# Kernel tuning notes

Measured on AMD Instinct MI355X. Metric: run time of the kernel, lower is better.

The kernel has to match this reference:

```python
import jax, jax.numpy as jnp
import numpy as np

NH = 12
D = 768
HD = D // NH
F = 3072
EPS = 1e-6
SCALE = 1.0 / np.sqrt(HD).astype(np.float32)


def _ln(x, g, b):
    m = x.mean(-1, keepdims=True)
    v = ((x - m) ** 2).mean(-1, keepdims=True)
    return (x - m) / jnp.sqrt(v + EPS) * g + b


def _heads(t):
    B, S, _ = t.shape
    return t.reshape(B, S, NH, HD).transpose(0, 2, 1, 3)  # [B,H,S,hd]


def _attn(q, k, v):
    # q,k,v: [B,H,S,hd]; dropout rate is 0 so omitted
    s = jnp.einsum('bhqd,bhkd->bhqk', q, k) * SCALE
    p = jax.nn.softmax(s, axis=-1)
    c = jnp.einsum('bhqk,bhkd->bhqd', p, v)
    B, H, S, _ = c.shape
    return c.transpose(0, 2, 1, 3).reshape(B, S, D)


def _mlp(x, W1, b1, W2, b2):
    h = jax.nn.gelu(x @ W1 + b1)  # dropout rate 0.1 -> identity (eval)
    return h @ W2 + b2


def setup_inputs() -> dict:
    key = jax.random.key(0)
    ks = jax.random.split(key, 16)
    B, S = 4, 1024
    rnd = lambda k, sh: (jax.random.normal(k, sh, jnp.float32) * 0.02)
    inp = {
        'x': jax.random.normal(ks[0], (B, S, D), jnp.float32),
        'y': jax.random.normal(ks[1], (B, S, D), jnp.float32),
        'ln1x_g': jnp.ones((D,)), 'ln1x_b': jnp.zeros((D,)),
        'ln1y_g': jnp.ones((D,)), 'ln1y_b': jnp.zeros((D,)),
        'Wq': rnd(ks[2], (D, D)), 'bq': jnp.zeros((D,)),
        'Wk': rnd(ks[3], (D, D)), 'bk': jnp.zeros((D,)),
        'Wv': rnd(ks[4], (D, D)), 'bv': jnp.zeros((D,)),
        'Wo': rnd(ks[5], (D, D)), 'bo': jnp.zeros((D,)),
        'Wqd': rnd(ks[6], (D, D)), 'bqd': jnp.zeros((D,)),
        'Wkd': rnd(ks[7], (D, D)), 'bkd': jnp.zeros((D,)),
        'Wvd': rnd(ks[8], (D, D)), 'bvd': jnp.zeros((D,)),
        'Wod': rnd(ks[9], (D, D)), 'bod': jnp.zeros((D,)),
        'w11': jnp.full((1,), 0.5), 'w12': jnp.full((1,), 0.5),
        'w21': jnp.full((1,), 0.5), 'w22': jnp.full((1,), 0.5),
        'ln2x_g': jnp.ones((D,)), 'ln2x_b': jnp.zeros((D,)),
        'ln2y_g': jnp.ones((D,)), 'ln2y_b': jnp.zeros((D,)),
        'W1': rnd(ks[10], (D, F)), 'b1': jnp.zeros((F,)),
        'W2': rnd(ks[11], (F, D)), 'b2': jnp.zeros((D,)),
        'W1d': rnd(ks[12], (D, F)), 'b1d': jnp.zeros((F,)),
        'W2d': rnd(ks[13], (F, D)), 'b2d': jnp.zeros((D,)),
    }
    return inp


def reference(x, y, ln1x_g, ln1x_b, ln1y_g, ln1y_b,
              Wq, bq, Wk, bk, Wv, bv, Wo, bo,
              Wqd, bqd, Wkd, bkd, Wvd, bvd, Wod, bod,
              w11, w12, w21, w22,
              ln2x_g, ln2x_b, ln2y_g, ln2y_b,
              W1, b1, W2, b2, W1d, b1d, W2d, b2d):
    hx, hy = x, y
    xn = _ln(x, ln1x_g, ln1x_b)
    yn = _ln(y, ln1y_g, ln1y_b)
    q = _heads(xn @ Wq + bq); k = _heads(xn @ Wk + bk); v = _heads(xn @ Wv + bv)
    qd = _heads(yn @ Wqd + bqd); kd = _heads(yn @ Wkd + bkd); vd = _heads(yn @ Wvd + bvd)
    a_sx = _attn(q, k, v) @ Wo + bo          # self-x
    a_sy = _attn(qd, kd, vd) @ Wod + bod     # self-y
    a_cx = _attn(q, kd, vd) @ Wo + bo        # cross x-query into y
    a_cy = _attn(qd, k, v) @ Wod + bod       # cross y-query into x
    ax = w11 * a_sx + w12 * a_cx
    ay = w21 * a_sy + w22 * a_cy
    x = ax + hx
    y = ay + hy
    hx, hy = x, y
    x = _mlp(_ln(x, ln2x_g, ln2x_b), W1, b1, W2, b2) + hx
    y = _mlp(_ln(y, ln2y_g, ln2y_b), W1d, b1d, W2d, b2d) + hy
    return (x, y)
```

## Files before the change

kernel.cpp:

```cpp
#include <hip/hip_runtime.h>

typedef unsigned short u16;
typedef unsigned short u16x8 __attribute__((ext_vector_type(8)));
typedef short s16x8 __attribute__((ext_vector_type(8)));
typedef float f32x4 __attribute__((ext_vector_type(4)));

#define EL ((size_t)3145728)
#define DDE ((size_t)589824)
#define DFE ((size_t)2359296)

#if __has_builtin(__builtin_amdgcn_exp2f)
#define EXP2(x) __builtin_amdgcn_exp2f(x)
#else
#define EXP2(x) __expf((x) * 0.6931471805599453f)
#endif

__device__ __forceinline__ float b2f(u16 u) {
    return __builtin_bit_cast(float, (unsigned)u << 16);
}
__device__ __forceinline__ u16 f2bf(float f) {
    unsigned x = __builtin_bit_cast(unsigned, f);
    return (u16)((x + 0x7fffu + ((x >> 16) & 1u)) >> 16);
}
__device__ __forceinline__ float gelu_f(float x) {
    float t = x + 0.044715f * x * x * x;
    return x * __builtin_amdgcn_rcpf(1.0f + EXP2(-2.302207417f * t));
}
__device__ __forceinline__ f32x4 mfma16(s16x8 a, s16x8 b, f32x4 c) {
    return __builtin_amdgcn_mfma_f32_16x16x32_bf16(a, b, c, 0, 0, 0);
}
__device__ __forceinline__ void gld16(const u16* g, u16* l) {
    __builtin_amdgcn_global_load_lds((const __attribute__((address_space(1))) void*)g,
                                     (__attribute__((address_space(3))) void*)l,
                                     16, 0, 0);
}
__device__ __forceinline__ void xcd_map(int NN, int& m, int& n, int& z) {
    int p = blockIdx.x, T = gridDim.x;
    int ppx = T >> 3;
    int xcd = p & 7, l = p >> 3;
    int panel = l / NN;
    n = l - panel * NN;
    int gp = xcd * (ppx / NN) + panel;
    z = gp >> 5;
    m = gp & 31;
}

__global__ __launch_bounds__(256) void transpose8_k(const float* p0, const float* p1,
                                                    const float* p2, const float* p3,
                                                    const float* p4, const float* p5,
                                                    const float* p6, const float* p7,
                                                    u16* __restrict__ dst0) {
    int z = blockIdx.z;
    const float* in = z == 0 ? p0 : z == 1 ? p1 : z == 2 ? p2 : z == 3 ? p3
                    : z == 4 ? p4 : z == 5 ? p5 : z == 6 ? p6 : p7;
    u16* out = dst0 + (size_t)z * DDE;
    const int K = 768, N = 768;
    __shared__ u16 tile[64][72];
    int k0 = blockIdx.y << 6, n0 = blockIdx.x << 6;
    int tid = threadIdx.x;
    int r = tid >> 2, c = (tid & 3) << 4;
    const float* ip = in + (size_t)(k0 + r) * N + n0 + c;
#pragma unroll
    for (int q = 0; q < 4; ++q) {
        f32x4 v = *(const f32x4*)(ip + 4 * q);
#pragma unroll
        for (int e = 0; e < 4; ++e) tile[r][c + 4 * q + e] = f2bf(v[e]);
    }
    __syncthreads();
    u16x8 o0, o1;
#pragma unroll
    for (int e = 0; e < 8; ++e) { o0[e] = tile[c + e][r]; o1[e] = tile[c + 8 + e][r]; }
    u16* op = out + (size_t)(n0 + r) * K + k0 + c;
    *(u16x8*)op = o0;
    *(u16x8*)(op + 8) = o1;
}

__global__ __launch_bounds__(256) void transpose2_k(const float* pa, const float* pb,
                                                    u16* __restrict__ dst0, size_t dsz,
                                                    int K, int N) {
    int z = blockIdx.z;
    const float* in = z ? pb : pa;
    u16* out = dst0 + (size_t)z * dsz;
    __shared__ u16 tile[64][72];
    int k0 = blockIdx.y << 6, n0 = blockIdx.x << 6;
    int tid = threadIdx.x;
    int r = tid >> 2, c = (tid & 3) << 4;
    const float* ip = in + (size_t)(k0 + r) * N + n0 + c;
#pragma unroll
    for (int q = 0; q < 4; ++q) {
        f32x4 v = *(const f32x4*)(ip + 4 * q);
#pragma unroll
        for (int e = 0; e < 4; ++e) tile[r][c + 4 * q + e] = f2bf(v[e]);
    }
    __syncthreads();
    u16x8 o0, o1;
#pragma unroll
    for (int e = 0; e < 8; ++e) { o0[e] = tile[c + e][r]; o1[e] = tile[c + 8 + e][r]; }
    u16* op = out + (size_t)(n0 + r) * K + k0 + c;
    *(u16x8*)op = o0;
    *(u16x8*)(op + 8) = o1;
}

__global__ __launch_bounds__(256) void ln_k(const float* __restrict__ inX,
                                            const float* __restrict__ inY,
                                            const float* gX, const float* bX,
                                            const float* gY, const float* bY,
                                            u16* __restrict__ out0) {
    int z = blockIdx.y;
    const float* in = z ? inY : inX;
    const float* g = z ? gY : gX;
    const float* be = z ? bY : bX;
    u16* out = out0 + (size_t)z * EL;
    int row = blockIdx.x, tid = threadIdx.x;
    const float* p = in + (size_t)row * 768;
    float v0 = p[tid], v1 = p[tid + 256], v2 = p[tid + 512];
    float s = v0 + v1 + v2;
    float q = v0 * v0 + v1 * v1 + v2 * v2;
#pragma unroll
    for (int m = 1; m < 64; m <<= 1) { s += __shfl_xor(s, m); q += __shfl_xor(q, m); }
    __shared__ float red[8];
    int w = tid >> 6, lane = tid & 63;
    if (lane == 0) { red[w] = s; red[4 + w] = q; }
    __syncthreads();
    s = red[0] + red[1] + red[2] + red[3];
    q = red[4] + red[5] + red[6] + red[7];
    float mean = s * (1.0f / 768.0f);
    float var = q * (1.0f / 768.0f) - mean * mean;
    float rstd = rsqrtf(var + 1e-6f);
    u16* o = out + (size_t)row * 768;
    o[tid]       = f2bf((v0 - mean) * rstd * g[tid]       + be[tid]);
    o[tid + 256] = f2bf((v1 - mean) * rstd * g[tid + 256] + be[tid + 256]);
    o[tid + 512] = f2bf((v2 - mean) * rstd * g[tid + 512] + be[tid + 512]);
}

__global__ __launch_bounds__(256) void lnb_k(const u16* __restrict__ inX,
                                             const u16* __restrict__ inY,
                                             const float* gX, const float* bX,
                                             const float* gY, const float* bY,
                                             u16* __restrict__ out0) {
    int z = blockIdx.y;
    const u16* in = z ? inY : inX;
    const float* g = z ? gY : gX;
    const float* be = z ? bY : bX;
    u16* out = out0 + (size_t)z * EL;
    int row = blockIdx.x, tid = threadIdx.x;
    const u16* p = in + (size_t)row * 768;
    float v0 = b2f(p[tid]), v1 = b2f(p[tid + 256]), v2 = b2f(p[tid + 512]);
    float s = v0 + v1 + v2;
    float q = v0 * v0 + v1 * v1 + v2 * v2;
#pragma unroll
    for (int m = 1; m < 64; m <<= 1) { s += __shfl_xor(s, m); q += __shfl_xor(q, m); }
    __shared__ float red[8];
    int w = tid >> 6, lane = tid & 63;
    if (lane == 0) { red[w] = s; red[4 + w] = q; }
    __syncthreads();
    s = red[0] + red[1] + red[2] + red[3];
    q = red[4] + red[5] + red[6] + red[7];
    float mean = s * (1.0f / 768.0f);
    float var = q * (1.0f / 768.0f) - mean * mean;
    float rstd = rsqrtf(var + 1e-6f);
    u16* o = out + (size_t)row * 768;
    o[tid]       = f2bf((v0 - mean) * rstd * g[tid]       + be[tid]);
    o[tid + 256] = f2bf((v1 - mean) * rstd * g[tid + 256] + be[tid + 256]);
    o[tid + 512] = f2bf((v2 - mean) * rstd * g[tid + 512] + be[tid + 512]);
}

__global__ __launch_bounds__(256) void blend_k(u16* __restrict__ a0,
                                               const u16* __restrict__ b0,
                                               const float* w11, const float* w12,
                                               const float* w21, const float* w22,
                                               int n8) {
    int z = blockIdx.z;
    u16* a = a0 + (size_t)z * EL;
    const u16* b = b0 + (size_t)z * EL;
    float wa = z ? *w21 : *w11, wb = z ? *w22 : *w12;
    for (int i = blockIdx.x * blockDim.x + threadIdx.x; i < n8;
         i += gridDim.x * blockDim.x) {
        u16x8 va = ((const u16x8*)a)[i];
        u16x8 vb = ((const u16x8*)b)[i];
        u16x8 r;
#pragma unroll
        for (int e = 0; e < 8; ++e) r[e] = f2bf(wa * b2f(va[e]) + wb * b2f(vb[e]));
        ((u16x8*)a)[i] = r;
    }
}

#define EPI_GELU 3
#define EPI_WO 4
#define EPI_MLP2 5

template <int EPI>
__global__ __launch_bounds__(256) void gemm_k(
    const u16* __restrict__ A0, size_t Asz,
    const u16* __restrict__ B0, size_t Bsz,
    const float* __restrict__ bias0, const float* __restrict__ bias1,
    const void* __restrict__ r0, const void* __restrict__ r1,
    const float* s1a, const float* s1b, const float* s2a, const float* s2b,
    void* __restrict__ C0, size_t Csz,
    int M, int N, int K, int NN) {
    int m_, n_, z;
    xcd_map(NN, m_, n_, z);
    const u16* A = A0 + z * Asz;
    const u16* BT = B0 + z * Bsz;
    const float* bias = z ? bias1 : bias0;
    const float* residf = (const float*)(z ? r1 : r0);
    const u16* residb = (const u16*)(z ? r1 : r0);
    u16* Cb = (u16*)C0 + z * Csz;
    float* Cf = (float*)C0 + z * Csz;
    __shared__ u16 lA[2][4096];
    __shared__ u16 lB[2][4096];
    int tid = threadIdx.x;
    int bm0 = m_ << 7, bn0 = n_ << 7;
    int lane = tid & 63, wid = tid >> 6;
    int fr = lane & 15, g = lane >> 4;
    int wm = wid >> 1, wn = wid & 1;
    const u16* srcA0 = A + (size_t)(bm0 + (tid & 127)) * K + ((tid >> 7) << 3);
    const u16* srcA1 = srcA0 + 16;
    const u16* srcB0 = BT + (size_t)(bn0 + (tid & 127)) * K + ((tid >> 7) << 3);
    const u16* srcB1 = srcB0 + 16;
    auto STAGE = [&](int buf, int k0) {
        gld16(srcA0 + k0, &lA[buf][0] + tid * 8);
        gld16(srcA1 + k0, &lA[buf][0] + 2048 + tid * 8);
        gld16(srcB0 + k0, &lB[buf][0] + tid * 8);
        gld16(srcB1 + k0, &lB[buf][0] + 2048 + tid * 8);
    };
    f32x4 acc[4][4] = {};
    STAGE(0, 0);
    __syncthreads();
    int cur = 0;
    for (int k0 = 0; k0 < K; k0 += 32) {
        if (k0 + 32 < K) STAGE(cur ^ 1, k0 + 32);
        s16x8 af[4], bf[4];
#pragma unroll
        for (int i = 0; i < 4; ++i)
            af[i] = *(const s16x8*)&lA[cur][(g * 128 + wm * 64 + i * 16 + fr) * 8];
#pragma unroll
        for (int j = 0; j < 4; ++j)
            bf[j] = *(const s16x8*)&lB[cur][(g * 128 + wn * 64 + j * 16 + fr) * 8];
#pragma unroll
        for (int i = 0; i < 4; ++i)
#pragma unroll
            for (int j = 0; j < 4; ++j)
                acc[i][j] = mfma16(af[i], bf[j], acc[i][j]);
        __syncthreads();
        cur ^= 1;
    }
    float bscale = 1.0f;
    if (EPI == EPI_WO) bscale = z ? (s2a[0] + s2b[0]) : (s1a[0] + s1b[0]);
#pragma unroll
    for (int j = 0; j < 4; ++j) {
        int n = bn0 + wn * 64 + j * 16 + fr;
        float bv = bias[n] * bscale;
#pragma unroll
        for (int i = 0; i < 4; ++i) {
#pragma unroll
            for (int r = 0; r < 4; ++r) {
                int m = bm0 + wm * 64 + i * 16 + (g << 2) + r;
                size_t idx = (size_t)m * N + n;
                float v = acc[i][j][r] + bv;
                if (EPI == EPI_GELU) {
                    Cb[idx] = f2bf(gelu_f(v));
                } else if (EPI == EPI_WO) {
                    Cb[idx] = f2bf(v + residf[idx]);
                } else {
                    Cf[idx] = v + b2f(residb[idx]);
                }
            }
        }
    }
}

__global__ __launch_bounds__(256) void gemm_qkv_k(const u16* __restrict__ A0,
                                                  const u16* __restrict__ B0,
                                                  const float* bq, const float* bk,
                                                  const float* bv, const float* bqd,
                                                  const float* bkd, const float* bvd,
                                                  u16* __restrict__ Qd,
                                                  u16* __restrict__ Kd,
                                                  u16* __restrict__ Vd) {
    const int K = 768;
    int m_, n_, z;
    xcd_map(18, m_, n_, z);
    const u16* A = A0 + z * EL;
    const u16* BT = B0 + z * 3 * DDE;
    __shared__ u16 lA[2][4096];
    __shared__ u16 lB[2][4096];
    int tid = threadIdx.x;
    int bm0 = m_ << 7, bn0 = n_ << 7;
    int lane = tid & 63, wid = tid >> 6, wm = wid >> 1, wn = wid & 1;
    int fr = lane & 15, g = lane >> 4;
    const u16* srcA0 = A + (size_t)(bm0 + (tid & 127)) * K + ((tid >> 7) << 3);
    const u16* srcA1 = srcA0 + 16;
    const u16* srcB0 = BT + (size_t)(bn0 + (tid & 127)) * K + ((tid >> 7) << 3);
    const u16* srcB1 = srcB0 + 16;
    auto STAGE = [&](int buf, int k0) {
        gld16(srcA0 + k0, &lA[buf][0] + tid * 8);
        gld16(srcA1 + k0, &lA[buf][0] + 2048 + tid * 8);
        gld16(srcB0 + k0, &lB[buf][0] + tid * 8);
        gld16(srcB1 + k0, &lB[buf][0] + 2048 + tid * 8);
    };
    f32x4 acc[4][4] = {};
    STAGE(0, 0);
    __syncthreads();
    int cur = 0;
    for (int k0 = 0; k0 < K; k0 += 32) {
        if (k0 + 32 < K) STAGE(cur ^ 1, k0 + 32);
        s16x8 af[4], bf[4];
#pragma unroll
        for (int i = 0; i < 4; ++i)
            af[i] = *(const s16x8*)&lA[cur][(g * 128 + wm * 64 + i * 16 + fr) * 8];
#pragma unroll
        for (int j = 0; j < 4; ++j)
            bf[j] = *(const s16x8*)&lB[cur][(g * 128 + wn * 64 + j * 16 + fr) * 8];
#pragma unroll
        for (int i = 0; i < 4; ++i)
#pragma unroll
            for (int j = 0; j < 4; ++j)
                acc[i][j] = mfma16(af[i], bf[j], acc[i][j]);
        __syncthreads();
        cur ^= 1;
    }
    int seg = bn0 / 768;
    const float* bp = seg == 0 ? (z ? bqd : bq) : seg == 1 ? (z ? bkd : bk) : (z ? bvd : bv);
    u16* out = (seg == 0 ? Qd : seg == 1 ? Kd : Vd) + (size_t)z * 3 * EL;
    int nbase = bn0 - seg * 768;
    const float qs = 0.180336880f;
#pragma unroll
    for (int j = 0; j < 4; ++j) {
        int nn = nbase + wn * 64 + j * 16 + fr;
        float bvl = bp[nn];
        int hh = nn >> 6, hd = nn & 63;
#pragma unroll
        for (int i = 0; i < 4; ++i) {
#pragma unroll
            for (int r = 0; r < 4; ++r) {
                int m = bm0 + wm * 64 + i * 16 + (g << 2) + r;
                int bb = m >> 10, ss = m & 1023;
                size_t o = ((size_t)(bb * 12 + hh)) << 16;
                if (seg < 2) o += ((size_t)ss << 6) + hd;
                else         o += ((size_t)hd << 10) + ss;
                float v = acc[i][j][r] + bvl;
                if (seg == 0) v *= qs;
                out[o] = f2bf(v);
            }
        }
    }
}

__global__ __launch_bounds__(256) void attn_k(const u16* __restrict__ Qx,
                                              const u16* __restrict__ Kx,
                                              const u16* __restrict__ VTx,
                                              const u16* __restrict__ Qy,
                                              const u16* __restrict__ Ky,
                                              const u16* __restrict__ VTy,
                                              u16* __restrict__ csx,
                                              u16* __restrict__ ccx,
                                              u16* __restrict__ csy,
                                              u16* __restrict__ ccy) {
    int p = blockIdx.x;
    int lg = (p & 7) * 192 + (p >> 3);
    int sg = lg >> 4, wi = lg & 15;
    int qt = wi & 7, sub = wi >> 3;
    int pairi = sg / 48, bh = sg % 48;
    int cfg = pairi == 0 ? (sub ? 3 : 0) : (sub ? 2 : 1);
    const u16 *Qp, *Kp, *Vp;
    u16* Op;
    if (cfg == 0)      { Qp = Qx; Kp = Kx; Vp = VTx; Op = csx; }
    else if (cfg == 1) { Qp = Qy; Kp = Ky; Vp = VTy; Op = csy; }
    else if (cfg == 2) { Qp = Qx; Kp = Ky; Vp = VTy; Op = ccx; }
    else               { Qp = Qy; Kp = Kx; Vp = VTx; Op = ccy; }
    const u16* Qh = Qp + ((size_t)bh << 16);
    const u16* Kh = Kp + ((size_t)bh << 16);
    const u16* Vh = Vp + ((size_t)bh << 16);
    int b = bh / 12, h = bh % 12;
    int tid = threadIdx.x, lane = tid & 63, w = tid >> 6;
    int q0 = qt * 128 + w * 32;
    int fr = lane & 15, ko = (lane >> 4) << 3, g = lane >> 4;
    bool glo = lane < 32;
    int srcA = fr + ((lane & 16) << 1);
    int srcB = srcA + 16;

    __shared__ u16 kls[2048];
    __shared__ u16 vls[2048];

    s16x8 qf[2][2];
#pragma unroll
    for (int s = 0; s < 2; ++s) {
        const u16* qp = Qh + (size_t)(q0 + s * 16 + fr) * 64 + ko;
        qf[s][0] = *(const s16x8*)qp;
        qf[s][1] = *(const s16x8*)(qp + 32);
    }

    f32x4 acc[2][4] = {};
    float lsum[2] = {0.f, 0.f};
    f32x4 zz = {0.f, 0.f, 0.f, 0.f};

    int krow = tid >> 3, kpc = tid & 7;
    int kgc = kpc ^ (krow & 7);
    int vdr = tid >> 2, vpv = tid & 3;
    int cK0 = ((fr << 3) + (g ^ (fr & 7))) << 3;
    int cK1 = ((fr << 3) + ((g + 4) ^ (fr & 7))) << 3;
    int cK2 = (((fr + 16) << 3) + (g ^ (fr & 7))) << 3;
    int cK3 = (((fr + 16) << 3) + ((g + 4) ^ (fr & 7))) << 3;

    for (int kb = 0; kb < 1024; kb += 32) {
        gld16(Kh + (size_t)(kb + krow) * 64 + kgc * 8, &kls[tid * 8]);
        gld16(Vh + (size_t)vdr * 1024 + kb + vpv * 8, &vls[tid * 8]);
        __syncthreads();
        s16x8 Kf0 = *(const s16x8*)&kls[cK0];
        s16x8 Kf1 = *(const s16x8*)&kls[cK1];
        s16x8 Kf2 = *(const s16x8*)&kls[cK2];
        s16x8 Kf3 = *(const s16x8*)&kls[cK3];
        s16x8 Vf[4];
#pragma unroll
        for (int t4 = 0; t4 < 4; ++t4)
            Vf[t4] = *(const s16x8*)&vls[((t4 * 16 + fr) << 5) + (g << 3)];
        s16x8 pa[2];
#pragma unroll
        for (int s = 0; s < 2; ++s) {
            __builtin_amdgcn_s_setprio(1);
            f32x4 t0 = mfma16(Kf0, qf[s][0], zz);
            t0 = mfma16(Kf1, qf[s][1], t0);
            f32x4 t1 = mfma16(Kf2, qf[s][0], zz);
            t1 = mfma16(Kf3, qf[s][1], t1);
            __builtin_amdgcn_s_setprio(0);
            float p00 = EXP2(t0[0]), p01 = EXP2(t0[1]);
            float p02 = EXP2(t0[2]), p03 = EXP2(t0[3]);
            float p10 = EXP2(t1[0]), p11 = EXP2(t1[1]);
            float p12 = EXP2(t1[2]), p13 = EXP2(t1[3]);
            lsum[s] += (p00 + p01 + p02 + p03) + (p10 + p11 + p12 + p13);
            unsigned w0, w1, w2, w3;
            asm("v_cvt_pk_bf16_f32 %0, %1, %2" : "=v"(w0) : "v"(p00), "v"(p01));
            asm("v_cvt_pk_bf16_f32 %0, %1, %2" : "=v"(w1) : "v"(p02), "v"(p03));
            asm("v_cvt_pk_bf16_f32 %0, %1, %2" : "=v"(w2) : "v"(p10), "v"(p11));
            asm("v_cvt_pk_bf16_f32 %0, %1, %2" : "=v"(w3) : "v"(p12), "v"(p13));
            int e0 = __shfl((int)w0, srcA), e1 = __shfl((int)w1, srcA);
            int e2 = __shfl((int)w0, srcB), e3 = __shfl((int)w1, srcB);
            int f0 = __shfl((int)w2, srcA), f1 = __shfl((int)w3, srcA);
            int f2 = __shfl((int)w2, srcB), f3 = __shfl((int)w3, srcB);
            int4 wd;
            wd.x = glo ? e0 : f0;
            wd.y = glo ? e1 : f1;
            wd.z = glo ? e2 : f2;
            wd.w = glo ? e3 : f3;
            pa[s] = __builtin_bit_cast(s16x8, wd);
        }
        __builtin_amdgcn_s_setprio(1);
#pragma unroll
        for (int t4 = 0; t4 < 4; ++t4) {
            acc[0][t4] = mfma16(pa[0], Vf[t4], acc[0][t4]);
            acc[1][t4] = mfma16(pa[1], Vf[t4], acc[1][t4]);
        }
        __builtin_amdgcn_s_setprio(0);
        __syncthreads();
    }

    float invv[2][4];
#pragma unroll
    for (int s = 0; s < 2; ++s) {
        float l = lsum[s];
        l += __shfl_xor(l, 16);
        l += __shfl_xor(l, 32);
        float inv = 1.0f / l;
#pragma unroll
        for (int r = 0; r < 4; ++r)
            invv[s][r] = __shfl(inv, ((lane >> 4) << 2) + r);
    }
#pragma unroll
    for (int s = 0; s < 2; ++s) {
        u16* ob = Op + (size_t)(b * 1024 + q0 + s * 16 + ((lane >> 4) << 2)) * 768 + h * 64 + fr;
#pragma unroll
        for (int t4 = 0; t4 < 4; ++t4)
#pragma unroll
            for (int r = 0; r < 4; ++r)
                ob[(size_t)r * 768 + t4 * 16] = f2bf(acc[s][t4][r] * invv[s][r]);
    }
}

extern "C" void kernel_launch(void* const* d_in, const int* in_sizes, int n_in,
                              void* d_out, int out_size, void* d_ws, size_t ws_size,
                              hipStream_t stream) {
    (void)in_sizes; (void)n_in; (void)out_size; (void)ws_size;
    const float* X    = (const float*)d_in[0];
    const float* Y    = (const float*)d_in[1];
    const float* l1xg = (const float*)d_in[2];
    const float* l1xb = (const float*)d_in[3];
    const float* l1yg = (const float*)d_in[4];
    const float* l1yb = (const float*)d_in[5];
    const float* Wq   = (const float*)d_in[6];
    const float* bq   = (const float*)d_in[7];
    const float* Wk   = (const float*)d_in[8];
    const float* bk   = (const float*)d_in[9];
    const float* Wv   = (const float*)d_in[10];
    const float* bv   = (const float*)d_in[11];
    const float* Wo   = (const float*)d_in[12];
    const float* bo   = (const float*)d_in[13];
    const float* Wqd  = (const float*)d_in[14];
    const float* bqd  = (const float*)d_in[15];
    const float* Wkd  = (const float*)d_in[16];
    const float* bkd  = (const float*)d_in[17];
    const float* Wvd  = (const float*)d_in[18];
    const float* bvd  = (const float*)d_in[19];
    const float* Wod  = (const float*)d_in[20];
    const float* bod  = (const float*)d_in[21];
    const float* w11  = (const float*)d_in[22];
    const float* w12  = (const float*)d_in[23];
    const float* w21  = (const float*)d_in[24];
    const float* w22  = (const float*)d_in[25];
    const float* l2xg = (const float*)d_in[26];
    const float* l2xb = (const float*)d_in[27];
    const float* l2yg = (const float*)d_in[28];
    const float* l2yb = (const float*)d_in[29];
    const float* W1   = (const float*)d_in[30];
    const float* b1   = (const float*)d_in[31];
    const float* W2   = (const float*)d_in[32];
    const float* b2   = (const float*)d_in[33];
    const float* W1d  = (const float*)d_in[34];
    const float* b1d  = (const float*)d_in[35];
    const float* W2d  = (const float*)d_in[36];
    const float* b2d  = (const float*)d_in[37];

    u16* ws = (u16*)d_ws;
    u16* qkvT = ws;
    u16* WoT  = qkvT + 6 * DDE;
    u16* W1T  = WoT + 2 * DDE;
    u16* W2T  = W1T + 2 * DFE;
    u16* xn   = W2T + 2 * DFE;
    u16* Qx   = xn + 2 * EL;
    u16* cs   = Qx + 6 * EL;
    u16* x1   = cs + 4 * EL;
    u16* Kx = Qx + EL;
    u16* VTx = Qx + 2 * EL;
    u16* Qy = Qx + 3 * EL;
    u16* Ky = Qx + 4 * EL;
    u16* VTy = Qx + 5 * EL;
    u16* h = Qx;
    u16* y1 = x1 + EL;

    float* out_x = (float*)d_out;

    dim3 tb(256);
    transpose8_k<<<dim3(12, 12, 8), tb, 0, stream>>>(Wq, Wk, Wv, Wqd, Wkd, Wvd, Wo, Wod, qkvT);
    transpose2_k<<<dim3(48, 12, 2), tb, 0, stream>>>(W1, W1d, W1T, DFE, 768, 3072);
    transpose2_k<<<dim3(12, 48, 2), tb, 0, stream>>>(W2, W2d, W2T, DFE, 3072, 768);
    ln_k<<<dim3(4096, 2), tb, 0, stream>>>(X, Y, l1xg, l1xb, l1yg, l1yb, xn);
    gemm_qkv_k<<<1152, tb, 0, stream>>>(xn, qkvT, bq, bk, bv, bqd, bkd, bvd,
                                        Qx, Kx, VTx);
    attn_k<<<4 * 48 * 8, tb, 0, stream>>>(Qx, Kx, VTx, Qy, Ky, VTy,
                                          cs, cs + 2 * EL, cs + EL, cs + 3 * EL);
    int n8 = (int)(EL / 8);
    blend_k<<<dim3(1536, 1, 2), tb, 0, stream>>>(cs, cs + 2 * EL, w11, w12, w21, w22, n8);
    gemm_k<EPI_WO><<<384, tb, 0, stream>>>(
        cs, EL, WoT, DDE, bo, bod, X, Y, w11, w12, w21, w22, x1, EL,
        4096, 768, 768, 6);
    lnb_k<<<dim3(4096, 2), tb, 0, stream>>>(x1, y1, l2xg, l2xb, l2yg, l2yb, xn);
    gemm_k<EPI_GELU><<<1536, tb, 0, stream>>>(
        xn, EL, W1T, DFE, b1, b1d, nullptr, nullptr, nullptr, nullptr, nullptr, nullptr,
        h, 4 * EL, 4096, 3072, 768, 24);
    gemm_k<EPI_MLP2><<<384, tb, 0, stream>>>(
        h, 4 * EL, W2T, DFE, b2, b2d, x1, y1, nullptr, nullptr, nullptr, nullptr,
        out_x, EL, 4096, 768, 3072, 6);
}
```

Before: 437.9 us.

## Split-K the second MLP GEMM with atomic accumulation into pre-initialized output

The final MLP down-projection (K=3072) was launched with only 384 blocks. It is now split four ways along K into 1536 blocks that add partial results into the fp32 output with atomics. The LayerNorm kernel now also writes the residual plus the b2 bias into that output so the atomics start from the right value. The aim is better CU occupancy on the tall-K GEMM, at the cost of atomic traffic, an extra fp32 write in the LN kernel, and a summation order that is no longer deterministic.

New measurement: 462.4 us. +5.6%, slower.

```diff
diff --git a/kernel.cpp b/kernel.cpp
--- a/kernel.cpp
+++ b/kernel.cpp
@@ -34,15 +34,16 @@
                                      (__attribute__((address_space(3))) void*)l,
                                      16, 0, 0);
 }
-__device__ __forceinline__ void xcd_map(int NN, int& m, int& n, int& z) {
+__device__ __forceinline__ void xcd_map(int NN, int& m, int& n, int& z, int& ks) {
     int p = blockIdx.x, T = gridDim.x;
     int ppx = T >> 3;
     int xcd = p & 7, l = p >> 3;
     int panel = l / NN;
     n = l - panel * NN;
     int gp = xcd * (ppx / NN) + panel;
-    z = gp >> 5;
     m = gp & 31;
+    z = (gp >> 5) & 1;
+    ks = gp >> 6;
 }
 
 __global__ __launch_bounds__(256) void transpose8_k(const float* p0, const float* p1,
@@ -133,16 +134,20 @@
     o[tid + 512] = f2bf((v2 - mean) * rstd * g[tid + 512] + be[tid + 512]);
 }
 
-__global__ __launch_bounds__(256) void lnb_k(const u16* __restrict__ inX,
-                                             const u16* __restrict__ inY,
-                                             const float* gX, const float* bX,
-                                             const float* gY, const float* bY,
-                                             u16* __restrict__ out0) {
+__global__ __launch_bounds__(256) void lnb_init_k(const u16* __restrict__ inX,
+                                                  const u16* __restrict__ inY,
+                                                  const float* gX, const float* bX,
+                                                  const float* gY, const float* bY,
+                                                  const float* b2X, const float* b2Y,
+                                                  u16* __restrict__ out0,
+                                                  float* __restrict__ outF0) {
     int z = blockIdx.y;
     const u16* in = z ? inY : inX;
     const float* g = z ? gY : gX;
     const float* be = z ? bY : bX;
+    const float* bb = z ? b2Y : b2X;
     u16* out = out0 + (size_t)z * EL;
+    float* of = outF0 + (size_t)z * EL;
     int row = blockIdx.x, tid = threadIdx.x;
     const u16* p = in + (size_t)row * 768;
     float v0 = b2f(p[tid]), v1 = b2f(p[tid + 256]), v2 = b2f(p[tid + 512]);
@@ -160,9 +165,13 @@
     float var = q * (1.0f / 768.0f) - mean * mean;
     float rstd = rsqrtf(var + 1e-6f);
     u16* o = out + (size_t)row * 768;
+    float* f = of + (size_t)row * 768;
     o[tid]       = f2bf((v0 - mean) * rstd * g[tid]       + be[tid]);
     o[tid + 256] = f2bf((v1 - mean) * rstd * g[tid + 256] + be[tid + 256]);
     o[tid + 512] = f2bf((v2 - mean) * rstd * g[tid + 512] + be[tid + 512]);
+    f[tid]       = v0 + bb[tid];
+    f[tid + 256] = v1 + bb[tid + 256];
+    f[tid + 512] = v2 + bb[tid + 512];
 }
 
 __global__ __launch_bounds__(256) void blend_k(u16* __restrict__ a0,
@@ -187,7 +196,7 @@
 
 #define EPI_GELU 3
 #define EPI_WO 4
-#define EPI_MLP2 5
+#define EPI_SK 5
 
 template <int EPI>
 __global__ __launch_bounds__(256) void gemm_k(
@@ -197,14 +206,14 @@
     const void* __restrict__ r0, const void* __restrict__ r1,
     const float* s1a, const float* s1b, const float* s2a, const float* s2b,
     void* __restrict__ C0, size_t Csz,
-    int M, int N, int K, int NN) {
-    int m_, n_, z;
-    xcd_map(NN, m_, n_, z);
+    int M, int N, int K, int NN, int KS) {
+    int m_, n_, z, ks;
+    xcd_map(NN, m_, n_, z, ks);
+    const int Kloc = K / KS;
     const u16* A = A0 + z * Asz;
     const u16* BT = B0 + z * Bsz;
     const float* bias = z ? bias1 : bias0;
     const float* residf = (const float*)(z ? r1 : r0);
-    const u16* residb = (const u16*)(z ? r1 : r0);
     u16* Cb = (u16*)C0 + z * Csz;
     float* Cf = (float*)C0 + z * Csz;
     __shared__ u16 lA[2][4096];
@@ -214,9 +223,9 @@
     int lane = tid & 63, wid = tid >> 6;
     int fr = lane & 15, g = lane >> 4;
     int wm = wid >> 1, wn = wid & 1;
-    const u16* srcA0 = A + (size_t)(bm0 + (tid & 127)) * K + ((tid >> 7) << 3);
+    const u16* srcA0 = A + (size_t)(bm0 + (tid & 127)) * K + ks * Kloc + ((tid >> 7) << 3);
     const u16* srcA1 = srcA0 + 16;
-    const u16* srcB0 = BT + (size_t)(bn0 + (tid & 127)) * K + ((tid >> 7) << 3);
+    const u16* srcB0 = BT + (size_t)(bn0 + (tid & 127)) * K + ks * Kloc + ((tid >> 7) << 3);
     const u16* srcB1 = srcB0 + 16;
     auto STAGE = [&](int buf, int k0) {
         gld16(srcA0 + k0, &lA[buf][0] + tid * 8);
@@ -228,8 +237,8 @@
     STAGE(0, 0);
     __syncthreads();
     int cur = 0;
-    for (int k0 = 0; k0 < K; k0 += 32) {
-        if (k0 + 32 < K) STAGE(cur ^ 1, k0 + 32);
+    for (int k0 = 0; k0 < Kloc; k0 += 32) {
+        if (k0 + 32 < Kloc) STAGE(cur ^ 1, k0 + 32);
         s16x8 af[4], bf[4];
 #pragma unroll
         for (int i = 0; i < 4; ++i)
@@ -250,7 +259,8 @@
 #pragma unroll
     for (int j = 0; j < 4; ++j) {
         int n = bn0 + wn * 64 + j * 16 + fr;
-        float bv = bias[n] * bscale;
+        float bv = 0.0f;
+        if (EPI != EPI_SK) bv = bias[n] * bscale;
 #pragma unroll
         for (int i = 0; i < 4; ++i) {
 #pragma unroll
@@ -263,7 +273,7 @@
                 } else if (EPI == EPI_WO) {
                     Cb[idx] = f2bf(v + residf[idx]);
                 } else {
-                    Cf[idx] = v + b2f(residb[idx]);
+                    unsafeAtomicAdd(&Cf[idx], v);
                 }
             }
         }
@@ -279,8 +289,8 @@
                                                   u16* __restrict__ Kd,
                                                   u16* __restrict__ Vd) {
     const int K = 768;
-    int m_, n_, z;
-    xcd_map(18, m_, n_, z);
+    int m_, n_, z, ks_;
+    xcd_map(18, m_, n_, z, ks_);
     const u16* A = A0 + z * EL;
     const u16* BT = B0 + z * 3 * DDE;
     __shared__ u16 lA[2][4096];
@@ -552,12 +562,14 @@
     blend_k<<<dim3(1536, 1, 2), tb, 0, stream>>>(cs, cs + 2 * EL, w11, w12, w21, w22, n8);
     gemm_k<EPI_WO><<<384, tb, 0, stream>>>(
         cs, EL, WoT, DDE, bo, bod, X, Y, w11, w12, w21, w22, x1, EL,
-        4096, 768, 768, 6);
-    lnb_k<<<dim3(4096, 2), tb, 0, stream>>>(x1, y1, l2xg, l2xb, l2yg, l2yb, xn);
+        4096, 768, 768, 6, 1);
+    lnb_init_k<<<dim3(4096, 2), tb, 0, stream>>>(x1, y1, l2xg, l2xb, l2yg, l2yb,
+                                                 b2, b2d, xn, out_x);
     gemm_k<EPI_GELU><<<1536, tb, 0, stream>>>(
         xn, EL, W1T, DFE, b1, b1d, nullptr, nullptr, nullptr, nullptr, nullptr, nullptr,
-        h, 4 * EL, 4096, 3072, 768, 24);
-    gemm_k<EPI_MLP2><<<384, tb, 0, stream>>>(
-        h, 4 * EL, W2T, DFE, b2, b2d, x1, y1, nullptr, nullptr, nullptr, nullptr,
-        out_x, EL, 4096, 768, 3072, 6);
-}
+        h, 4 * EL, 4096, 3072, 768, 24, 1);
+    gemm_k<EPI_SK><<<1536, tb, 0, stream>>>(
+        h, 4 * EL, W2T, DFE, nullptr, nullptr, nullptr, nullptr,
+        nullptr, nullptr, nullptr, nullptr,
+        out_x, EL, 4096, 768, 3072, 6, 4);
+}
```

## Double-buffer attention K/V tiles and stage V-transpose stores through LDS

Applied to the files above, without the earlier changes.

The attention loop now loads 64-key chunks into double-buffered LDS, prefetching the next chunk while the current one is computed, which halves the number of barriers. The V tile in LDS gets an XOR swizzle to reduce bank conflicts. The QKV GEMM epilogue for the V segment transposes through shared memory so that it writes 16-byte coalesced stores instead of scattered 2-byte stores. LDS use per block rises in attention (32KB), which may lower occupancy. xcd_map also gains an unused k-split output, and z is now masked to one bit.

Result: faster. 417.0 us (-4.8%).

```diff
diff --git a/kernel.cpp b/kernel.cpp
--- a/kernel.cpp
+++ b/kernel.cpp
@@ -34,15 +34,16 @@
                                      (__attribute__((address_space(3))) void*)l,
                                      16, 0, 0);
 }
-__device__ __forceinline__ void xcd_map(int NN, int& m, int& n, int& z) {
+__device__ __forceinline__ void xcd_map(int NN, int& m, int& n, int& z, int& ks) {
     int p = blockIdx.x, T = gridDim.x;
     int ppx = T >> 3;
     int xcd = p & 7, l = p >> 3;
     int panel = l / NN;
     n = l - panel * NN;
     int gp = xcd * (ppx / NN) + panel;
-    z = gp >> 5;
     m = gp & 31;
+    z = (gp >> 5) & 1;
+    ks = gp >> 6;
 }
 
 __global__ __launch_bounds__(256) void transpose8_k(const float* p0, const float* p1,
@@ -198,8 +199,8 @@
     const float* s1a, const float* s1b, const float* s2a, const float* s2b,
     void* __restrict__ C0, size_t Csz,
     int M, int N, int K, int NN) {
-    int m_, n_, z;
-    xcd_map(NN, m_, n_, z);
+    int m_, n_, z, ks;
+    xcd_map(NN, m_, n_, z, ks);
     const u16* A = A0 + z * Asz;
     const u16* BT = B0 + z * Bsz;
     const float* bias = z ? bias1 : bias0;
@@ -279,12 +280,11 @@
                                                   u16* __restrict__ Kd,
                                                   u16* __restrict__ Vd) {
     const int K = 768;
-    int m_, n_, z;
-    xcd_map(18, m_, n_, z);
+    int m_, n_, z, ks_;
+    xcd_map(18, m_, n_, z, ks_);
     const u16* A = A0 + z * EL;
     const u16* BT = B0 + z * 3 * DDE;
-    __shared__ u16 lA[2][4096];
-    __shared__ u16 lB[2][4096];
+    __shared__ u16 lsm[4][4096];
     int tid = threadIdx.x;
     int bm0 = m_ << 7, bn0 = n_ << 7;
     int lane = tid & 63, wid = tid >> 6, wm = wid >> 1, wn = wid & 1;
@@ -294,10 +294,10 @@
     const u16* srcB0 = BT + (size_t)(bn0 + (tid & 127)) * K + ((tid >> 7) << 3);
     const u16* srcB1 = srcB0 + 16;
     auto STAGE = [&](int buf, int k0) {
-        gld16(srcA0 + k0, &lA[buf][0] + tid * 8);
-        gld16(srcA1 + k0, &lA[buf][0] + 2048 + tid * 8);
-        gld16(srcB0 + k0, &lB[buf][0] + tid * 8);
-        gld16(srcB1 + k0, &lB[buf][0] + 2048 + tid * 8);
+        gld16(srcA0 + k0, &lsm[buf][0] + tid * 8);
+        gld16(srcA1 + k0, &lsm[buf][0] + 2048 + tid * 8);
+        gld16(srcB0 + k0, &lsm[2 + buf][0] + tid * 8);
+        gld16(srcB1 + k0, &lsm[2 + buf][0] + 2048 + tid * 8);
     };
     f32x4 acc[4][4] = {};
     STAGE(0, 0);
@@ -308,10 +308,10 @@
         s16x8 af[4], bf[4];
 #pragma unroll
         for (int i = 0; i < 4; ++i)
-            af[i] = *(const s16x8*)&lA[cur][(g * 128 + wm * 64 + i * 16 + fr) * 8];
+            af[i] = *(const s16x8*)&lsm[cur][(g * 128 + wm * 64 + i * 16 + fr) * 8];
 #pragma unroll
         for (int j = 0; j < 4; ++j)
-            bf[j] = *(const s16x8*)&lB[cur][(g * 128 + wn * 64 + j * 16 + fr) * 8];
+            bf[j] = *(const s16x8*)&lsm[2 + cur][(g * 128 + wn * 64 + j * 16 + fr) * 8];
 #pragma unroll
         for (int i = 0; i < 4; ++i)
 #pragma unroll
@@ -322,27 +322,57 @@
     }
     int seg = bn0 / 768;
     const float* bp = seg == 0 ? (z ? bqd : bq) : seg == 1 ? (z ? bkd : bk) : (z ? bvd : bv);
-    u16* out = (seg == 0 ? Qd : seg == 1 ? Kd : Vd) + (size_t)z * 3 * EL;
     int nbase = bn0 - seg * 768;
-    const float qs = 0.180336880f;
-#pragma unroll
-    for (int j = 0; j < 4; ++j) {
-        int nn = nbase + wn * 64 + j * 16 + fr;
-        float bvl = bp[nn];
-        int hh = nn >> 6, hd = nn & 63;
-#pragma unroll
-        for (int i = 0; i < 4; ++i) {
-#pragma unroll
-            for (int r = 0; r < 4; ++r) {
-                int m = bm0 + wm * 64 + i * 16 + (g << 2) + r;
-                int bb = m >> 10, ss = m & 1023;
-                size_t o = ((size_t)(bb * 12 + hh)) << 16;
-                if (seg < 2) o += ((size_t)ss << 6) + hd;
-                else         o += ((size_t)hd << 10) + ss;
-                float v = acc[i][j][r] + bvl;
-                if (seg == 0) v *= qs;
-                out[o] = f2bf(v);
+    if (seg < 2) {
+        u16* out = (seg == 0 ? Qd : Kd);
+        size_t zoff = (size_t)z * 3 * EL;
+        const float qs = (seg == 0) ? 0.180336880f : 1.0f;
+#pragma unroll
+        for (int j = 0; j < 4; ++j) {
+            int nn = nbase + wn * 64 + j * 16 + fr;
+            float bvl = bp[nn];
+            int hh = nn >> 6, hd = nn & 63;
+#pragma unroll
+            for (int i = 0; i < 4; ++i) {
+#pragma unroll
+                for (int r = 0; r < 4; ++r) {
+                    int m = bm0 + wm * 64 + i * 16 + (g << 2) + r;
+                    int bb = m >> 10, ss = m & 1023;
+                    size_t o = zoff + (((size_t)(bb * 12 + hh)) << 16)
+                             + ((size_t)ss << 6) + hd;
+                    out[o] = f2bf((acc[i][j][r] + bvl) * qs);
+                }
             }
+        }
+    } else {
+        u16* tbuf = &lsm[0][0];
+#pragma unroll
+        for (int j = 0; j < 4; ++j) {
+            int nl = wn * 64 + j * 16 + fr;
+            float bvl = bp[nbase + nl];
+#pragma unroll
+            for (int i = 0; i < 4; ++i) {
+#pragma unroll
+                for (int r = 0; r < 4; ++r) {
+                    int sl = wm * 64 + i * 16 + (g << 2) + r;
+                    tbuf[sl * 128 + nl] = f2bf(acc[i][j][r] + bvl);
+                }
+            }
+        }
+        __syncthreads();
+        int dl = tid >> 1;
+        int sb = (tid & 1) * 64;
+        int dg = nbase + dl;
+        int hh = dg >> 6, hd = dg & 63;
+        int bb = bm0 >> 10;
+        size_t obase = (size_t)z * 3 * EL + (((size_t)(bb * 12 + hh)) << 16)
+                     + ((size_t)hd << 10) + (bm0 & 1023) + sb;
+#pragma unroll
+        for (int c = 0; c < 64; c += 8) {
+            u16x8 v;
+#pragma unroll
+            for (int e = 0; e < 8; ++e) v[e] = tbuf[(sb + c + e) * 128 + dl];
+            *(u16x8*)(Vd + obase + c) = v;
         }
     }
 }
@@ -380,8 +410,8 @@
     int srcA = fr + ((lane & 16) << 1);
     int srcB = srcA + 16;
 
-    __shared__ u16 kls[2048];
-    __shared__ u16 vls[2048];
+    __shared__ u16 kls[8192];
+    __shared__ u16 vls[8192];
 
     s16x8 qf[2][2];
 #pragma unroll
@@ -398,23 +428,30 @@
     int krow = tid >> 3, kpc = tid & 7;
     int kgc = kpc ^ (krow & 7);
     int vdr = tid >> 2, vpv = tid & 3;
+    int vgc = vpv ^ ((vdr >> 1) & 3);
     int cK0 = ((fr << 3) + (g ^ (fr & 7))) << 3;
     int cK1 = ((fr << 3) + ((g + 4) ^ (fr & 7))) << 3;
     int cK2 = (((fr + 16) << 3) + (g ^ (fr & 7))) << 3;
     int cK3 = (((fr + 16) << 3) + ((g + 4) ^ (fr & 7))) << 3;
-
-    for (int kb = 0; kb < 1024; kb += 32) {
-        gld16(Kh + (size_t)(kb + krow) * 64 + kgc * 8, &kls[tid * 8]);
-        gld16(Vh + (size_t)vdr * 1024 + kb + vpv * 8, &vls[tid * 8]);
-        __syncthreads();
-        s16x8 Kf0 = *(const s16x8*)&kls[cK0];
-        s16x8 Kf1 = *(const s16x8*)&kls[cK1];
-        s16x8 Kf2 = *(const s16x8*)&kls[cK2];
-        s16x8 Kf3 = *(const s16x8*)&kls[cK3];
+    int cVg = (g ^ ((fr >> 1) & 3)) << 3;
+
+    auto STAGE = [&](int buf, int kb) {
+        int lb = buf * 4096 + tid * 8;
+        gld16(Kh + (size_t)(kb + krow) * 64 + kgc * 8, &kls[lb]);
+        gld16(Kh + (size_t)(kb + 32 + krow) * 64 + kgc * 8, &kls[lb + 2048]);
+        gld16(Vh + (size_t)vdr * 1024 + kb + vgc * 8, &vls[lb]);
+        gld16(Vh + (size_t)vdr * 1024 + kb + 32 + vgc * 8, &vls[lb + 2048]);
+    };
+
+    auto HALF = [&](int base) {
+        s16x8 Kf0 = *(const s16x8*)&kls[base + cK0];
+        s16x8 Kf1 = *(const s16x8*)&kls[base + cK1];
+        s16x8 Kf2 = *(const s16x8*)&kls[base + cK2];
+        s16x8 Kf3 = *(const s16x8*)&kls[base + cK3];
         s16x8 Vf[4];
 #pragma unroll
         for (int t4 = 0; t4 < 4; ++t4)
-            Vf[t4] = *(const s16x8*)&vls[((t4 * 16 + fr) << 5) + (g << 3)];
+            Vf[t4] = *(const s16x8*)&vls[base + ((t4 * 16 + fr) << 5) + cVg];
         s16x8 pa[2];
 #pragma unroll
         for (int s = 0; s < 2; ++s) {
@@ -452,7 +489,16 @@
             acc[1][t4] = mfma16(pa[1], Vf[t4], acc[1][t4]);
         }
         __builtin_amdgcn_s_setprio(0);
+    };
+
+    STAGE(0, 0);
+    int cur = 0;
+    for (int kb = 0; kb < 1024; kb += 64) {
         __syncthreads();
+        if (kb + 64 < 1024) STAGE(cur ^ 1, kb + 64);
+        HALF(cur * 4096);
+        HALF(cur * 4096 + 2048);
+        cur ^= 1;
     }
 
     float invv[2][4];
@@ -531,9 +577,6 @@
     u16* x1   = cs + 4 * EL;
     u16* Kx = Qx + EL;
     u16* VTx = Qx + 2 * EL;
-    u16* Qy = Qx + 3 * EL;
-    u16* Ky = Qx + 4 * EL;
-    u16* VTy = Qx + 5 * EL;
     u16* h = Qx;
     u16* y1 = x1 + EL;
 
@@ -546,7 +589,7 @@
     ln_k<<<dim3(4096, 2), tb, 0, stream>>>(X, Y, l1xg, l1xb, l1yg, l1yb, xn);
     gemm_qkv_k<<<1152, tb, 0, stream>>>(xn, qkvT, bq, bk, bv, bqd, bkd, bvd,
                                         Qx, Kx, VTx);
-    attn_k<<<4 * 48 * 8, tb, 0, stream>>>(Qx, Kx, VTx, Qy, Ky, VTy,
+    attn_k<<<4 * 48 * 8, tb, 0, stream>>>(Qx, Kx, VTx, Qx + 3 * EL, Qx + 4 * EL, Qx + 5 * EL,
                                           cs, cs + 2 * EL, cs + EL, cs + 3 * EL);
     int n8 = (int)(EL / 8);
     blend_k<<<dim3(1536, 1, 2), tb, 0, stream>>>(cs, cs + 2 * EL, w11, w12, w21, w22, n8);
```
